# Optimization experiments

Hardware: AMD Instinct MI355X
Metric: run time of the kernel (lower is better)

## Reference

```python
import jax, jax.numpy as jnp
import numpy as np

D_MODEL = 1024
NUM_HEADS = 16
HEAD_DIM = D_MODEL // NUM_HEADS


def setup_inputs() -> dict:
    key = jax.random.key(0)
    ks = jax.random.split(key, 9)
    s = D_MODEL ** -0.5  # roughly like nn.Linear init scale
    x = jax.random.normal(ks[0], (4, 2048, D_MODEL), dtype=jnp.float32)
    Wq = jax.random.normal(ks[1], (D_MODEL, D_MODEL), dtype=jnp.float32) * s
    bq = jax.random.normal(ks[2], (D_MODEL,), dtype=jnp.float32) * s
    Wk = jax.random.normal(ks[3], (D_MODEL, D_MODEL), dtype=jnp.float32) * s
    bk = jax.random.normal(ks[4], (D_MODEL,), dtype=jnp.float32) * s
    Wv = jax.random.normal(ks[5], (D_MODEL, D_MODEL), dtype=jnp.float32) * s
    bv = jax.random.normal(ks[6], (D_MODEL,), dtype=jnp.float32) * s
    Wo = jax.random.normal(ks[7], (D_MODEL, D_MODEL), dtype=jnp.float32) * s
    bo = jax.random.normal(ks[8], (D_MODEL,), dtype=jnp.float32) * s
    return {"x": x, "Wq": Wq, "bq": bq, "Wk": Wk, "bk": bk,
            "Wv": Wv, "bv": bv, "Wo": Wo, "bo": bo}


def reference(x, Wq, bq, Wk, bk, Wv, bv, Wo, bo):
    B, S, D = x.shape
    H, Dh = NUM_HEADS, HEAD_DIM
    scale = Dh ** -0.5
    # nn.Linear: x @ W.T + b
    q = (x @ Wq.T + bq).reshape(B, S, H, Dh)
    k = (x @ Wk.T + bk).reshape(B, S, H, Dh)
    v = (x @ Wv.T + bv).reshape(B, S, H, Dh)
    # scores: (B, H, S, S), full materialization as in the original bmm path
    dp = scale * jnp.einsum('bqhd,bkhd->bhqk', q, k)
    att = jax.nn.softmax(dp, axis=-1)
    out = jnp.einsum('bhqk,bkhd->bqhd', att, v).reshape(B, S, D)
    return out @ Wo.T + bo
```

## Files before the change

### kernel.cpp

```cpp
#include <hip/hip_runtime.h>
#include <stdint.h>

typedef __attribute__((ext_vector_type(8))) __bf16 bf16x8;
typedef __attribute__((ext_vector_type(4))) float floatx4;

#define DEV __device__ __forceinline__

DEV unsigned short f2bf(float f) {
    union { float f; unsigned u; } uf; uf.f = f;
    unsigned u = uf.u;
    unsigned r = (u + 0x7fffu + ((u >> 16) & 1u)) >> 16;
    return (unsigned short)r;
}

DEV float fast_exp2(float x) {
#if __has_builtin(__builtin_amdgcn_exp2f)
    return __builtin_amdgcn_exp2f(x);
#else
    return exp2f(x);
#endif
}

DEV unsigned pack_trunc2(float lo, float hi) {
    return __builtin_amdgcn_perm(__float_as_uint(hi), __float_as_uint(lo), 0x07060302u);
}

DEV void async16(const void* g, void* l) {
    __builtin_amdgcn_global_load_lds(
        (const __attribute__((address_space(1))) void*)g,
        (__attribute__((address_space(3))) void*)l, 16, 0, 0);
}

__global__ void cast_bf16_kernel(const float* __restrict__ src,
                                 unsigned short* __restrict__ dst, int n4) {
    int i = blockIdx.x * blockDim.x + threadIdx.x;
    if (i >= n4) return;
    float4 v = reinterpret_cast<const float4*>(src)[i];
    ushort4 o;
    o.x = f2bf(v.x); o.y = f2bf(v.y); o.z = f2bf(v.z); o.w = f2bf(v.w);
    reinterpret_cast<ushort4*>(dst)[i] = o;
}

__global__ void cast_w_kernel(const float* __restrict__ Wq, const float* __restrict__ Wk,
                              const float* __restrict__ Wv, const float* __restrict__ Wo,
                              const float* __restrict__ bq, const float* __restrict__ bk,
                              const float* __restrict__ bv,
                              unsigned short* __restrict__ wqkv,
                              unsigned short* __restrict__ wo,
                              float* __restrict__ bqkv) {
    const int NW = 262144;
    int i = blockIdx.x * blockDim.x + threadIdx.x;
    if (i < 4 * NW) {
        int seg = i >> 18, off = i & (NW - 1);
        const float* src = (seg == 0) ? Wq : (seg == 1) ? Wk : (seg == 2) ? Wv : Wo;
        unsigned short* dst = (seg < 3) ? (wqkv + seg * 1048576) : wo;
        float4 v = reinterpret_cast<const float4*>(src)[off];
        ushort4 o;
        o.x = f2bf(v.x); o.y = f2bf(v.y); o.z = f2bf(v.z); o.w = f2bf(v.w);
        reinterpret_cast<ushort4*>(dst)[off] = o;
    } else {
        int j = i - 4 * NW;
        if (j < 768) {
            int seg = j >> 8, off = j & 255;
            const float* src = (seg == 0) ? bq : (seg == 1) ? bk : bv;
            reinterpret_cast<float4*>(bqkv)[j] =
                reinterpret_cast<const float4*>(src)[off];
        }
    }
}

template <int MODE>
__global__ __launch_bounds__(256)
void gemm128(const unsigned short* __restrict__ A,
             const unsigned short* __restrict__ B,
             const float* __restrict__ bias,
             unsigned short* __restrict__ q_ws,
             unsigned short* __restrict__ k_ws,
             unsigned short* __restrict__ v_ws,
             float* __restrict__ fout) {
    constexpr int K = 1024;
    __shared__ alignas(16) unsigned short smem[128 * 136];
    unsigned short* sA = smem;
    unsigned short* sB = smem + 128 * 64;
    unsigned short* sT = smem;
    float* sT32 = reinterpret_cast<float*>(smem);

    const int tid = threadIdx.x;
    const int w = tid >> 6, lane = tid & 63, quad = lane >> 4, l16 = lane & 15;
    const int wr = w >> 1, wc = w & 1;
    const int bm = blockIdx.y, bn = blockIdx.x;
    const int arow0 = bm * 128, brow0 = bn * 128;

    floatx4 acc[4][4];
#pragma unroll
    for (int i = 0; i < 4; i++)
#pragma unroll
        for (int j = 0; j < 4; j++) acc[i][j] = (floatx4){0.f, 0.f, 0.f, 0.f};

    for (int k0 = 0; k0 < K; k0 += 64) {
#pragma unroll
        for (int i = 0; i < 4; i++) {
            int cb = i * 256 + w * 64;
            int ci = cb + lane;
            int row = ci >> 3, cl = ci & 7, cs = cl ^ (row & 7);
            async16(A + (size_t)(arow0 + row) * K + k0 + cs * 8, (char*)sA + cb * 16);
            async16(B + (size_t)(brow0 + row) * K + k0 + cs * 8, (char*)sB + cb * 16);
        }
        __syncthreads();
#pragma unroll
        for (int kk = 0; kk < 2; kk++) {
            bf16x8 aF[4], bF[4];
#pragma unroll
            for (int i = 0; i < 4; i++) {
                int row = wr * 64 + i * 16 + l16;
                int c = kk * 4 + quad, ph = c ^ (row & 7);
                aF[i] = *reinterpret_cast<const bf16x8*>(sA + row * 64 + ph * 8);
            }
#pragma unroll
            for (int j = 0; j < 4; j++) {
                int row = wc * 64 + j * 16 + l16;
                int c = kk * 4 + quad, ph = c ^ (row & 7);
                bF[j] = *reinterpret_cast<const bf16x8*>(sB + row * 64 + ph * 8);
            }
#pragma unroll
            for (int i = 0; i < 4; i++)
#pragma unroll
                for (int j = 0; j < 4; j++)
                    acc[i][j] = __builtin_amdgcn_mfma_f32_16x16x32_bf16(
                        aF[i], bF[j], acc[i][j], 0, 0, 0);
        }
        __syncthreads();
    }

    if (MODE == 1) {
#pragma unroll
        for (int ch = 0; ch < 2; ch++) {
            if (ch) __syncthreads();
            if (wr == ch) {
#pragma unroll
                for (int j = 0; j < 4; j++) {
                    const int c = wc * 64 + j * 16 + l16;
                    const float bia = bias[brow0 + c];
#pragma unroll
                    for (int i = 0; i < 4; i++) {
                        int s_loc = i * 16 + quad * 4;
#pragma unroll
                        for (int r = 0; r < 4; r++)
                            sT32[(s_loc + r) * 132 + c] = acc[i][j][r] + bia;
                    }
                }
            }
            __syncthreads();
            const int cpos = (tid & 31) * 4;
#pragma unroll
            for (int it = 0; it < 8; it++) {
                int s_loc = (tid >> 5) + it * 8;
                int grow = arow0 + ch * 64 + s_loc;
                float4 vv = *reinterpret_cast<const float4*>(sT32 + s_loc * 132 + cpos);
                *reinterpret_cast<float4*>(fout + (size_t)grow * 1024 + brow0 + cpos) = vv;
            }
        }
    } else if (bn < 16) {
        unsigned short* dst = (bn < 8) ? q_ws : k_ws;
        const float sc = (bn < 8) ? 0.18033688f : 1.0f;
#pragma unroll
        for (int j = 0; j < 4; j++) {
            const int c = wc * 64 + j * 16 + l16;
            const float bia = bias[brow0 + c];
#pragma unroll
            for (int i = 0; i < 4; i++) {
                int s_loc = wr * 64 + i * 16 + quad * 4;
#pragma unroll
                for (int r = 0; r < 4; r++)
                    sT[(s_loc + r) * 136 + c] = f2bf((acc[i][j][r] + bia) * sc);
            }
        }
        __syncthreads();
        const int nnbase = (bn & 7) * 128;
        const int c0 = (tid & 15) * 8;
        const int h = (nnbase + c0) >> 6, d = c0 & 63;
#pragma unroll
        for (int it = 0; it < 8; it++) {
            int s_loc = (tid >> 4) + it * 16;
            int s = arow0 + s_loc;
            int bb = s >> 11, s4 = s & 2047;
            uint4 vdat = *reinterpret_cast<const uint4*>(sT + s_loc * 136 + c0);
            *reinterpret_cast<uint4*>(
                dst + ((size_t)(bb * 16 + h) * 2048 + s4) * 64 + d) = vdat;
        }
    } else {
#pragma unroll
        for (int j = 0; j < 4; j++) {
            const int c = wc * 64 + j * 16 + l16;
            const float bia = bias[brow0 + c];
#pragma unroll
            for (int i = 0; i < 4; i++) {
                int v_hi = wr * 4 + i;
#pragma unroll
                for (int r = 0; r < 4; r++) {
                    int v = (quad * 4 + r) * 8 + v_hi;
                    sT[c * 136 + v] = f2bf(acc[i][j][r] + bia);
                }
            }
        }
        __syncthreads();
        const int bb = bm >> 4, blk = bm & 15;
        const int chunk = tid & 15;
#pragma unroll
        for (int it = 0; it < 8; it++) {
            int row = (tid >> 4) + it * 16;
            int h = (bn - 16) * 2 + (row >> 6), d = row & 63;
            ushort4 lo = *reinterpret_cast<const ushort4*>(sT + row * 136 + chunk * 8);
            ushort4 hi = *reinterpret_cast<const ushort4*>(sT + row * 136 + chunk * 8 + 4);
            size_t off = ((size_t)(bb * 16 + h) * 64 + d) * 2048 + blk * 128 + chunk * 8;
            *reinterpret_cast<ushort4*>(v_ws + off) = lo;
            *reinterpret_cast<ushort4*>(v_ws + off + 4) = hi;
        }
    }
}

__global__ __launch_bounds__(256)
void attn_kernel(const unsigned short* __restrict__ q_ws,
                 const unsigned short* __restrict__ k_ws,
                 const unsigned short* __restrict__ v_ws,
                 unsigned short* __restrict__ o_ws) {
    constexpr int PP = 152;
    __shared__ alignas(16) unsigned short sK[128 * 64];
    __shared__ alignas(16) unsigned short sVt[64 * 128];
    __shared__ alignas(16) unsigned short sP[4][16 * PP];

    const int tid = threadIdx.x;
    const int w = tid >> 6, lane = tid & 63, quad = lane >> 4, l16 = lane & 15;
    const int id = blockIdx.x;
    const int bh = (id >> 8) * 8 + (id & 7);
    const int q0 = ((id >> 3) & 31) * 64;
    const size_t base = (size_t)bh * 2048 * 64;

    bf16x8 aQ[2];
    {
        int qrow = q0 + w * 16 + l16;
        const unsigned short* qp = q_ws + base + (size_t)qrow * 64 + quad * 8;
        aQ[0] = *reinterpret_cast<const bf16x8*>(qp);
        aQ[1] = *reinterpret_cast<const bf16x8*>(qp + 32);
    }

    const unsigned short* kptr[4];
    const unsigned short* vptr[4];
    char* klds[4];
    char* vlds[4];
#pragma unroll
    for (int i = 0; i < 4; i++) {
        int cb = i * 256 + w * 64;
        int ci = cb + lane;
        {
            int row = ci >> 3, cl = ci & 7, cs = cl ^ (row & 7);
            kptr[i] = k_ws + base + (size_t)row * 64 + cs * 8;
            klds[i] = (char*)sK + cb * 16;
        }
        {
            int row = ci >> 4, cl = ci & 15, cs = cl ^ (row & 15);
            vptr[i] = v_ws + base + (size_t)row * 2048 + cs * 8;
            vlds[i] = (char*)sVt + cb * 16;
        }
    }

    const __bf16 one = (__bf16)1.0f;
    const bf16x8 vOnes = {one, one, one, one, one, one, one, one};

    floatx4 oAcc[4], rsAcc;
#pragma unroll
    for (int j = 0; j < 4; j++) oAcc[j] = (floatx4){0.f, 0.f, 0.f, 0.f};
    rsAcc = (floatx4){0.f, 0.f, 0.f, 0.f};

    for (int t = 0; t < 16; t++) {
        const int kv0 = t * 128;
#pragma unroll
        for (int i = 0; i < 4; i++) {
            async16(kptr[i] + (size_t)kv0 * 64, klds[i]);
            async16(vptr[i] + kv0, vlds[i]);
        }
        __syncthreads();

        floatx4 sAcc[8];
#pragma unroll
        for (int j = 0; j < 8; j++) sAcc[j] = (floatx4){0.f, 0.f, 0.f, 0.f};
#pragma unroll
        for (int kk = 0; kk < 2; kk++) {
#pragma unroll
            for (int j = 0; j < 8; j++) {
                int krow = j * 16 + l16;
                int c = kk * 4 + quad, ph = c ^ (krow & 7);
                bf16x8 bK = *reinterpret_cast<const bf16x8*>(sK + krow * 64 + ph * 8);
                sAcc[j] = __builtin_amdgcn_mfma_f32_16x16x32_bf16(aQ[kk], bK, sAcc[j], 0, 0, 0);
            }
        }

#pragma unroll
        for (int r = 0; r < 4; r++) {
            float e[8];
#pragma unroll
            for (int j = 0; j < 8; j++) e[j] = fast_exp2(sAcc[j][r]);
            uint4 pk;
            pk.x = pack_trunc2(e[0], e[1]);
            pk.y = pack_trunc2(e[2], e[3]);
            pk.z = pack_trunc2(e[4], e[5]);
            pk.w = pack_trunc2(e[6], e[7]);
            *reinterpret_cast<uint4*>(&sP[w][(quad * 4 + r) * PP + l16 * 8]) = pk;
        }
        asm volatile("s_waitcnt lgkmcnt(0)" ::: "memory");

        bf16x8 aP[4];
#pragma unroll
        for (int ks = 0; ks < 4; ks++)
            aP[ks] = *reinterpret_cast<const bf16x8*>(&sP[w][l16 * PP + ks * 32 + quad * 8]);
#pragma unroll
        for (int jd = 0; jd < 4; jd++) {
            int drow = jd * 16 + l16;
#pragma unroll
            for (int ks = 0; ks < 4; ks++) {
                int c = ks * 4 + quad, ph = c ^ (drow & 15);
                bf16x8 bV = *reinterpret_cast<const bf16x8*>(sVt + drow * 128 + ph * 8);
                oAcc[jd] = __builtin_amdgcn_mfma_f32_16x16x32_bf16(aP[ks], bV, oAcc[jd], 0, 0, 0);
            }
        }
#pragma unroll
        for (int ks = 0; ks < 4; ks++)
            rsAcc = __builtin_amdgcn_mfma_f32_16x16x32_bf16(aP[ks], vOnes, rsAcc, 0, 0, 0);
        __syncthreads();
    }

    float inv[4];
#pragma unroll
    for (int r = 0; r < 4; r++) inv[r] = 1.0f / rsAcc[r];
    const int bb = bh >> 4, h = bh & 15;
#pragma unroll
    for (int jd = 0; jd < 4; jd++) {
        int d = jd * 16 + l16;
#pragma unroll
        for (int r = 0; r < 4; r++) {
            int s = q0 + w * 16 + quad * 4 + r;
            float v = oAcc[jd][r] * inv[r];
            o_ws[((size_t)bb * 2048 + s) * 1024 + h * 64 + d] = f2bf(v);
        }
    }
}

extern "C" void kernel_launch(void* const* d_in, const int* in_sizes, int n_in,
                              void* d_out, int out_size, void* d_ws, size_t ws_size,
                              hipStream_t stream) {
    const float* x  = (const float*)d_in[0];
    const float* Wq = (const float*)d_in[1];
    const float* bq = (const float*)d_in[2];
    const float* Wk = (const float*)d_in[3];
    const float* bk = (const float*)d_in[4];
    const float* Wv = (const float*)d_in[5];
    const float* bv = (const float*)d_in[6];
    const float* Wo = (const float*)d_in[7];
    const float* bo = (const float*)d_in[8];
    float* out = (float*)d_out;

    char* ws = (char*)d_ws;
    unsigned short* xb   = (unsigned short*)(ws);
    unsigned short* wqkv = (unsigned short*)(ws + (16ull << 20));
    unsigned short* wo   = (unsigned short*)(ws + (22ull << 20));
    float*          bqkv = (float*)(ws + (24ull << 20));
    unsigned short* q_ws = (unsigned short*)(ws + (25ull << 20));
    unsigned short* k_ws = (unsigned short*)(ws + (41ull << 20));
    unsigned short* v_ws = (unsigned short*)(ws + (57ull << 20));
    unsigned short* o_ws = xb;

    const int n4x = 8192 * 1024 / 4;
    cast_bf16_kernel<<<n4x / 256, 256, 0, stream>>>(x, xb, n4x);
    cast_w_kernel<<<4099, 256, 0, stream>>>(Wq, Wk, Wv, Wo, bq, bk, bv,
                                            wqkv, wo, bqkv);

    gemm128<0><<<dim3(24, 64), 256, 0, stream>>>(xb, wqkv, bqkv, q_ws, k_ws, v_ws, nullptr);
    attn_kernel<<<2048, 256, 0, stream>>>(q_ws, k_ws, v_ws, o_ws);
    gemm128<1><<<dim3(8, 64), 256, 0, stream>>>(o_ws, wo, bo, nullptr, nullptr, nullptr, out);
}
```

Baseline: 298.5 us.

## Alias attention P buffer onto K smem, raise occupancy, swap GEMM grid order

The attention kernel drops its separate per-wave P scratch buffer and reuses the K tile region, behind an extra barrier and an XOR-swizzled layout, which shrinks LDS per block. Together with a launch bound of 5 blocks per SM, this aims for higher occupancy. The GEMM grids are transposed so consecutive blocks walk along M rather than N, which changes L2 reuse of weight tiles. The cost is an extra __syncthreads per KV tile and more register pressure from keeping all four packed P rows live.

Result: faster. 288.3 us (-3.4%).

```diff
diff --git a/kernel.cpp b/kernel.cpp
--- a/kernel.cpp
+++ b/kernel.cpp
@@ -88,7 +88,7 @@
     const int tid = threadIdx.x;
     const int w = tid >> 6, lane = tid & 63, quad = lane >> 4, l16 = lane & 15;
     const int wr = w >> 1, wc = w & 1;
-    const int bm = blockIdx.y, bn = blockIdx.x;
+    const int bm = blockIdx.x, bn = blockIdx.y;
     const int arow0 = bm * 128, brow0 = bn * 128;
 
     floatx4 acc[4][4];
@@ -219,15 +219,14 @@
     }
 }
 
-__global__ __launch_bounds__(256)
+__global__ __launch_bounds__(256, 5)
 void attn_kernel(const unsigned short* __restrict__ q_ws,
                  const unsigned short* __restrict__ k_ws,
                  const unsigned short* __restrict__ v_ws,
                  unsigned short* __restrict__ o_ws) {
-    constexpr int PP = 152;
-    __shared__ alignas(16) unsigned short sK[128 * 64];
-    __shared__ alignas(16) unsigned short sVt[64 * 128];
-    __shared__ alignas(16) unsigned short sP[4][16 * PP];
+    __shared__ alignas(16) unsigned short smem[2 * 128 * 64];
+    unsigned short* sK  = smem;
+    unsigned short* sVt = smem + 128 * 64;
 
     const int tid = threadIdx.x;
     const int w = tid >> 6, lane = tid & 63, quad = lane >> 4, l16 = lane & 15;
@@ -235,6 +234,8 @@
     const int bh = (id >> 8) * 8 + (id & 7);
     const int q0 = ((id >> 3) & 31) * 64;
     const size_t base = (size_t)bh * 2048 * 64;
+
+    unsigned short* sPw = smem + w * 2048;
 
     bf16x8 aQ[2];
     {
@@ -295,24 +296,31 @@
             }
         }
 
+        uint4 pk[4];
 #pragma unroll
         for (int r = 0; r < 4; r++) {
             float e[8];
 #pragma unroll
             for (int j = 0; j < 8; j++) e[j] = fast_exp2(sAcc[j][r]);
-            uint4 pk;
-            pk.x = pack_trunc2(e[0], e[1]);
-            pk.y = pack_trunc2(e[2], e[3]);
-            pk.z = pack_trunc2(e[4], e[5]);
-            pk.w = pack_trunc2(e[6], e[7]);
-            *reinterpret_cast<uint4*>(&sP[w][(quad * 4 + r) * PP + l16 * 8]) = pk;
+            pk[r].x = pack_trunc2(e[0], e[1]);
+            pk[r].y = pack_trunc2(e[2], e[3]);
+            pk[r].z = pack_trunc2(e[4], e[5]);
+            pk[r].w = pack_trunc2(e[6], e[7]);
+        }
+        __syncthreads();
+
+#pragma unroll
+        for (int r = 0; r < 4; r++) {
+            int row = quad * 4 + r;
+            *reinterpret_cast<uint4*>(sPw + row * 128 + ((l16 ^ row) & 15) * 8) = pk[r];
         }
         asm volatile("s_waitcnt lgkmcnt(0)" ::: "memory");
 
         bf16x8 aP[4];
 #pragma unroll
         for (int ks = 0; ks < 4; ks++)
-            aP[ks] = *reinterpret_cast<const bf16x8*>(&sP[w][l16 * PP + ks * 32 + quad * 8]);
+            aP[ks] = *reinterpret_cast<const bf16x8*>(
+                sPw + l16 * 128 + (((ks * 4 + quad) ^ l16) & 15) * 8);
 #pragma unroll
         for (int jd = 0; jd < 4; jd++) {
             int drow = jd * 16 + l16;
@@ -374,7 +382,7 @@
     cast_w_kernel<<<4099, 256, 0, stream>>>(Wq, Wk, Wv, Wo, bq, bk, bv,
                                             wqkv, wo, bqkv);
 
-    gemm128<0><<<dim3(24, 64), 256, 0, stream>>>(xb, wqkv, bqkv, q_ws, k_ws, v_ws, nullptr);
+    gemm128<0><<<dim3(64, 24), 256, 0, stream>>>(xb, wqkv, bqkv, q_ws, k_ws, v_ws, nullptr);
     attn_kernel<<<2048, 256, 0, stream>>>(q_ws, k_ws, v_ws, o_ws);
-    gemm128<1><<<dim3(8, 64), 256, 0, stream>>>(o_ws, wo, bo, nullptr, nullptr, nullptr, out);
-}
+    gemm128<1><<<dim3(64, 8), 256, 0, stream>>>(o_ws, wo, bo, nullptr, nullptr, nullptr, out);
+}
```
